# Kernel tuning notes

Hardware: AMD Instinct MI355X
Metric: run time of the kernel (lower is better)

The kernel has to match this reference:

```python
import jax, jax.numpy as jnp
import numpy as np

B, N, F_IN, F_HID, F_OUT = 32, 1024, 512, 512, 512


def setup_inputs() -> dict:
    key = jax.random.key(0)
    ks = jax.random.split(key, 8)
    def xavier(k, fan_in, fan_out):
        bound = float(np.sqrt(6.0 / (fan_in + fan_out)))
        return jax.random.uniform(k, (fan_in, fan_out), jnp.float32, -bound, bound)
    return {
        "batch_graph": jax.random.normal(ks[0], (B, N, F_IN), jnp.float32),
        "adj": jax.random.uniform(ks[1], (B, N, N), jnp.float32),
        "W1": xavier(ks[2], F_IN, F_HID),
        "b1": jnp.zeros((F_HID,), jnp.float32),
        "W2": xavier(ks[3], F_HID, F_HID),
        "b2": jnp.zeros((F_HID,), jnp.float32),
        "W3": xavier(ks[4], F_HID, F_OUT),
        "b3": jnp.zeros((F_OUT,), jnp.float32),
    }


def _gcn_layer(x, adj, W, b):
    # support = X @ W ; out = A @ support + b  (per graph in the batch)
    support = jnp.einsum("bnf,fh->bnh", x, W)
    return jnp.einsum("bnm,bmh->bnh", adj, support) + b


def reference(batch_graph, adj, W1, b1, W2, b2, W3, b3):
    # Block-diagonal big_adj @ big_graph is exactly a batched per-graph matmul:
    # the zero off-diagonal blocks contribute nothing, so math is identical.
    # Dropout is identity at inference (eval mode).
    x = jax.nn.relu(_gcn_layer(batch_graph, adj, W1, b1))
    x = jax.nn.relu(_gcn_layer(x, adj, W2, b2))
    out = _gcn_layer(x, adj, W3, b3)  # [B, N, F_OUT]
    return out
```

## Files before the change

kernel.cpp:

```cpp
#include <hip/hip_runtime.h>
#include <hip/hip_bf16.h>


typedef __attribute__((ext_vector_type(8))) short bf16x8s;
typedef __attribute__((ext_vector_type(4))) float f32x4;
typedef __attribute__((ext_vector_type(4))) unsigned short us4;
typedef __attribute__((ext_vector_type(8))) unsigned short us8;

__device__ __forceinline__ unsigned short f2bf(float f) {
    unsigned u = __builtin_bit_cast(unsigned, f);
    u += 0x7fffu + ((u >> 16) & 1u);
    return (unsigned short)(u >> 16);
}

__device__ __forceinline__ void async16(const unsigned short* g, unsigned short* l) {
    __builtin_amdgcn_global_load_lds(
        (const __attribute__((address_space(1))) unsigned int*)g,
        (__attribute__((address_space(3))) unsigned int*)l, 16, 0, 0);
}

#define MFMA_(d, va, vb) d = __builtin_amdgcn_mfma_f32_16x16x32_bf16(va, vb, d, 0, 0, 0)

__global__ void prep(const float* __restrict__ x0, unsigned short* __restrict__ P0, long n4,
                     const float* __restrict__ W1, const float* __restrict__ W2,
                     const float* __restrict__ W3, unsigned short* __restrict__ WT1,
                     unsigned short* __restrict__ WT2, unsigned short* __restrict__ WT3,
                     int F) {
    long i = (long)blockIdx.x * blockDim.x + threadIdx.x;
    long stride = (long)gridDim.x * blockDim.x;
    for (long k = i; k < n4; k += stride) {
        float4 v = ((const float4*)x0)[k];
        us4 o;
        o.x = f2bf(v.x); o.y = f2bf(v.y); o.z = f2bf(v.z); o.w = f2bf(v.w);
        ((us4*)P0)[k] = o;
    }
    const long FF = (long)F * F;
    for (long k = i; k < 3 * FF; k += stride) {
        int w = (int)(k / FF);
        long idx = k % FF;
        int r = (int)(idx % F);
        int c = (int)(idx / F);
        const float* W = (w == 0) ? W1 : (w == 1) ? W2 : W3;
        unsigned short* WT = (w == 0) ? WT1 : (w == 1) ? WT2 : WT3;
        WT[idx] = f2bf(W[(size_t)r * F + c]);
    }
}

__global__ void cvt_f32_bf16(const float* __restrict__ in, unsigned short* __restrict__ out, long n4) {
    long i = (long)blockIdx.x * blockDim.x + threadIdx.x;
    long stride = (long)gridDim.x * blockDim.x;
    for (; i < n4; i += stride) {
        float4 v = ((const float4*)in)[i];
        us4 o;
        o.x = f2bf(v.x); o.y = f2bf(v.y); o.z = f2bf(v.z); o.w = f2bf(v.w);
        ((us4*)out)[i] = o;
    }
}

template<bool RELU, bool OUT_F32>
__global__ __launch_bounds__(512, 2)
void gemm256(const unsigned short* __restrict__ A,
             const unsigned short* __restrict__ BT,
             void* __restrict__ Cout,
             const float* __restrict__ bias,
             int M, int N, int K,
             long sA, long sBT, long sC)
{
    __shared__ unsigned short Lraw[65536];

    const int t    = threadIdx.x;
    const int lane = t & 63;
    const int wv   = t >> 6;
    const int wm   = wv >> 2;
    const int wn   = wv & 3;
    const int fr   = lane & 15;
    const int fk   = (lane >> 4) * 8;
    const int r4   = (lane >> 4) * 4;

    const int tilesN = N >> 8;
    const int bpb    = (M >> 8) * tilesN;
    const int cpx = gridDim.x >> 3;
    const int lb  = (blockIdx.x & 7) * cpx + (blockIdx.x >> 3);
    const int bat = lb / bpb;
    const int tt  = lb % bpb;
    const int m0  = (tt / tilesN) << 8;
    const int n0  = (tt % tilesN) << 8;

    const unsigned short* Ab = A  + (size_t)bat * sA  + (size_t)m0 * K;
    const unsigned short* Bb = BT + (size_t)bat * sBT + (size_t)n0 * K;

    int srow[2], scol[2], lo[2];
#pragma unroll
    for (int r = 0; r < 2; ++r) {
        int c   = r * 512 + t;
        srow[r] = c >> 3;
        scol[r] = ((c & 7) * 8) ^ ((srow[r] & 7) << 3);
        lo[r]   = c * 8;
    }

    auto stageA = [&](int kt, int h) {
        unsigned short* base = Lraw + (kt & 1) * 16384;
#pragma unroll
        for (int r = 0; r < 2; ++r)
            async16(Ab + (size_t)(h * 128 + srow[r]) * K + kt * 64 + scol[r],
                    base + h * 8192 + lo[r]);
    };
    auto stageB = [&](int kt, int h) {
        unsigned short* base = Lraw + 32768 + (kt & 1) * 16384;
#pragma unroll
        for (int r = 0; r < 2; ++r)
            async16(Bb + (size_t)(h * 128 + srow[r]) * K + kt * 64 + scol[r],
                    base + h * 8192 + lo[r]);
    };
    auto rdA = [&](int buf, int mf, int kkj) -> bf16x8s {
        int row = wm * 128 + mf * 16 + fr;
        int e   = (kkj * 32 + fk) ^ ((row & 7) << 3);
        return *(const bf16x8s*)&Lraw[buf * 16384 + row * 64 + e];
    };
    auto rdB = [&](int buf, int nf, int kkj) -> bf16x8s {
        int row = wn * 64 + nf * 16 + fr;
        int e   = (kkj * 32 + fk) ^ ((row & 7) << 3);
        return *(const bf16x8s*)&Lraw[32768 + buf * 16384 + row * 64 + e];
    };

    const int nt = K >> 6;

    f32x4 acc[8][4];
#pragma unroll
    for (int i = 0; i < 8; ++i)
#pragma unroll
        for (int j = 0; j < 4; ++j) acc[i][j] = f32x4{0.f, 0.f, 0.f, 0.f};

    bf16x8s aP[4], aB[4], aC[4], bX[4], bY[4];

    stageA(0, 0); stageB(0, 0); stageA(0, 1); stageB(0, 1);
    asm volatile("s_waitcnt vmcnt(0)" ::: "memory");
    __builtin_amdgcn_s_barrier();
#pragma unroll
    for (int m = 0; m < 4; ++m) aP[m] = rdA(0, m, 0);
#pragma unroll
    for (int n = 0; n < 4; ++n) bX[n] = rdB(0, n, 0);

    for (int it = 0; it < nt; ++it) {
        const int cur  = it & 1;
        const int nxt  = cur ^ 1;
        const bool more = (it + 1 < nt);

        __builtin_amdgcn_s_barrier();
#pragma unroll
        for (int m = 0; m < 4; ++m) aB[m] = rdA(cur, m + 4, 0);
        if (more) { stageA(it + 1, 0); stageB(it + 1, 0); }
        __builtin_amdgcn_s_setprio(1);
#pragma unroll
        for (int m = 0; m < 4; ++m)
#pragma unroll
            for (int n = 0; n < 4; ++n) MFMA_(acc[m][n], aP[m], bX[n]);
        __builtin_amdgcn_s_setprio(0);

        __builtin_amdgcn_s_barrier();
#pragma unroll
        for (int m = 0; m < 4; ++m) aC[m] = rdA(cur, m, 1);
#pragma unroll
        for (int n = 0; n < 4; ++n) bY[n] = rdB(cur, n, 1);
        if (more) { stageA(it + 1, 1); stageB(it + 1, 1); }
        __builtin_amdgcn_s_setprio(1);
#pragma unroll
        for (int m = 0; m < 4; ++m)
#pragma unroll
            for (int n = 0; n < 4; ++n) MFMA_(acc[m + 4][n], aB[m], bX[n]);
        __builtin_amdgcn_s_setprio(0);

        __builtin_amdgcn_s_barrier();
#pragma unroll
        for (int m = 0; m < 4; ++m) aB[m] = rdA(cur, m + 4, 1);
        __builtin_amdgcn_s_setprio(1);
#pragma unroll
        for (int m = 0; m < 4; ++m)
#pragma unroll
            for (int n = 0; n < 4; ++n) MFMA_(acc[m][n], aC[m], bY[n]);
        __builtin_amdgcn_s_setprio(0);

        if (more) {
            asm volatile("s_waitcnt vmcnt(0)" ::: "memory");
            __builtin_amdgcn_s_barrier();
#pragma unroll
            for (int m = 0; m < 4; ++m) aP[m] = rdA(nxt, m, 0);
#pragma unroll
            for (int n = 0; n < 4; ++n) bX[n] = rdB(nxt, n, 0);
        }
        __builtin_amdgcn_s_setprio(1);
#pragma unroll
        for (int m = 0; m < 4; ++m)
#pragma unroll
            for (int n = 0; n < 4; ++n) MFMA_(acc[m + 4][n], aB[m], bY[n]);
        __builtin_amdgcn_s_setprio(0);
    }

    __syncthreads();

    const int R0 = m0 + wm * 128;
    const int C0 = n0 + wn * 64;
    float bv[4];
#pragma unroll
    for (int j = 0; j < 4; ++j)
        bv[j] = bias ? bias[C0 + j * 16 + fr] : 0.f;

    if (OUT_F32) {
        float* Cb = (float*)Cout + (size_t)bat * sC;
#pragma unroll
        for (int j = 0; j < 4; ++j)
#pragma unroll
            for (int i = 0; i < 8; ++i)
#pragma unroll
                for (int e = 0; e < 4; ++e) {
                    float v = acc[i][j][e] + bv[j];
                    if (RELU) v = fmaxf(v, 0.f);
                    Cb[(size_t)(R0 + i * 16 + r4 + e) * N + C0 + j * 16 + fr] = v;
                }
    } else {
        unsigned short* sl = Lraw + wv * 8192;
#pragma unroll
        for (int i = 0; i < 8; ++i)
#pragma unroll
            for (int j = 0; j < 4; ++j)
#pragma unroll
                for (int e = 0; e < 4; ++e) {
                    float v = acc[i][j][e] + bv[j];
                    if (RELU) v = fmaxf(v, 0.f);
                    const int row = i * 16 + r4 + e;
                    const int col = j * 16 + fr;
                    sl[row * 64 + (col ^ ((row & 7) << 3))] = f2bf(v);
                }
        unsigned short* Cb = (unsigned short*)Cout + (size_t)bat * sC;
#pragma unroll
        for (int rr = 0; rr < 16; ++rr) {
            const int row = rr * 8 + (lane >> 3);
            const int k8  = lane & 7;
            us8 v = *(const us8*)&sl[row * 64 + ((k8 ^ (row & 7)) << 3)];
            *(us8*)&Cb[(size_t)(R0 + row) * N + C0 + k8 * 8] = v;
        }
    }
}

extern "C" void kernel_launch(void* const* d_in, const int* in_sizes, int n_in,
                              void* d_out, int out_size, void* d_ws, size_t ws_size,
                              hipStream_t stream) {
    constexpr int B = 32, N = 1024, F = 512;

    const float* x0f  = (const float*)d_in[0];
    const float* adjf = (const float*)d_in[1];
    const float* W1 = (const float*)d_in[2];
    const float* b1 = (const float*)d_in[3];
    const float* W2 = (const float*)d_in[4];
    const float* b2 = (const float*)d_in[5];
    const float* W3 = (const float*)d_in[6];
    const float* b3 = (const float*)d_in[7];

    unsigned short* ws   = (unsigned short*)d_ws;
    unsigned short* adjb = ws;
    unsigned short* P0   = adjb + (size_t)B * N * N;
    unsigned short* P1   = P0 + (size_t)B * N * F;
    unsigned short* PT   = P1 + (size_t)B * N * F;
    unsigned short* WT1  = PT + (size_t)B * N * F;
    unsigned short* WT2  = WT1 + (size_t)F * F;
    unsigned short* WT3  = WT2 + (size_t)F * F;

    prep<<<2048, 256, 0, stream>>>(x0f, P0, (long)B * N * F / 4,
                                   W1, W2, W3, WT1, WT2, WT3, F);
    cvt_f32_bf16<<<2048, 256, 0, stream>>>(adjf, adjb, (long)B * N * N / 4);

    const int grid = 256;
    const long sX = (long)N * F;
    const long sAd = (long)N * N;

    gemm256<false, false><<<grid, 512, 0, stream>>>(WT1,  P0, PT, nullptr, F, N, F, 0,  sX, sX);
    gemm256<true,  false><<<grid, 512, 0, stream>>>(adjb, PT, P1, b1,      N, F, N, sAd, sX, sX);
    gemm256<false, false><<<grid, 512, 0, stream>>>(WT2,  P1, PT, nullptr, F, N, F, 0,  sX, sX);
    gemm256<true,  false><<<grid, 512, 0, stream>>>(adjb, PT, P0, b2,      N, F, N, sAd, sX, sX);
    gemm256<false, false><<<grid, 512, 0, stream>>>(WT3,  P0, PT, nullptr, F, N, F, 0,  sX, sX);
    gemm256<false, true ><<<grid, 512, 0, stream>>>(adjb, PT, (float*)d_out, b3, N, F, N, sAd, sX, sX);
}
```

Baseline: 256.3 us.

## Fuse all GCN layers and adj conversion into one persistent kernel with flag sync

Replaces the six GEMM launches and the separate adjacency conversion kernel with a single persistent 256-block kernel. Per-tile completion flags let each adj@support GEMM start consuming K-chunks as soon as the producing X@W tiles finish. The fp32-to-bf16 adjacency conversion is interleaved after the first X@W GEMM, and grid-wide barriers separate the layers. This aims to remove launch gaps and tail idle time and to overlap the conversion with compute. It relies on all 256 blocks being co-resident (2 per CU) to avoid deadlock, and it adds spin-wait and atomic overhead.

Measured after the change: 737.7 us. 188% more time.

```diff
diff --git a/kernel.cpp b/kernel.cpp
--- a/kernel.cpp
+++ b/kernel.cpp
@@ -20,6 +20,10 @@
 }
 
 #define MFMA_(d, va, vb) d = __builtin_amdgcn_mfma_f32_16x16x32_bf16(va, vb, d, 0, 0, 0)
+
+__global__ void zero_sync(unsigned* s, int n) {
+    for (int i = threadIdx.x; i < n; i += 256) s[i] = 0;
+}
 
 __global__ void prep(const float* __restrict__ x0, unsigned short* __restrict__ P0, long n4,
                      const float* __restrict__ W1, const float* __restrict__ W2,
@@ -46,28 +50,34 @@
     }
 }
 
-__global__ void cvt_f32_bf16(const float* __restrict__ in, unsigned short* __restrict__ out, long n4) {
-    long i = (long)blockIdx.x * blockDim.x + threadIdx.x;
-    long stride = (long)gridDim.x * blockDim.x;
-    for (; i < n4; i += stride) {
-        float4 v = ((const float4*)in)[i];
-        us4 o;
-        o.x = f2bf(v.x); o.y = f2bf(v.y); o.z = f2bf(v.z); o.w = f2bf(v.w);
-        ((us4*)out)[i] = o;
-    }
-}
-
-template<bool RELU, bool OUT_F32>
-__global__ __launch_bounds__(512, 2)
-void gemm256(const unsigned short* __restrict__ A,
-             const unsigned short* __restrict__ BT,
-             void* __restrict__ Cout,
-             const float* __restrict__ bias,
-             int M, int N, int K,
-             long sA, long sBT, long sC)
+__device__ __forceinline__ void waitge(unsigned* p, unsigned tgt, int t) {
+    if (t == 0) {
+        while (__hip_atomic_load(p, __ATOMIC_ACQUIRE, __HIP_MEMORY_SCOPE_AGENT) < tgt)
+            __builtin_amdgcn_s_sleep(2);
+    }
+    __syncthreads();
+    __builtin_amdgcn_sched_barrier(0);
+}
+
+__device__ __forceinline__ void gbar(unsigned* slot, unsigned nb, int t) {
+    __syncthreads();
+    if (t == 0) {
+        __hip_atomic_fetch_add(slot, 1u, __ATOMIC_ACQ_REL, __HIP_MEMORY_SCOPE_AGENT);
+        while (__hip_atomic_load(slot, __ATOMIC_ACQUIRE, __HIP_MEMORY_SCOPE_AGENT) < nb)
+            __builtin_amdgcn_s_sleep(2);
+    }
+    __syncthreads();
+    __builtin_amdgcn_sched_barrier(0);
+}
+
+__device__ __forceinline__ void gemm_core(
+    unsigned short* Lraw,
+    const unsigned short* __restrict__ A, const unsigned short* __restrict__ BT,
+    void* __restrict__ Cout, const float* __restrict__ bias,
+    int N, int K, int lgTN, long sA, long sBT, long sC,
+    bool relu, bool outf32,
+    unsigned* wTf, unsigned* wCvt, unsigned* sTf, int lb)
 {
-    __shared__ unsigned short Lraw[65536];
-
     const int t    = threadIdx.x;
     const int lane = t & 63;
     const int wv   = t >> 6;
@@ -77,14 +87,11 @@
     const int fk   = (lane >> 4) * 8;
     const int r4   = (lane >> 4) * 4;
 
-    const int tilesN = N >> 8;
-    const int bpb    = (M >> 8) * tilesN;
-    const int cpx = gridDim.x >> 3;
-    const int lb  = (blockIdx.x & 7) * cpx + (blockIdx.x >> 3);
-    const int bat = lb / bpb;
-    const int tt  = lb % bpb;
-    const int m0  = (tt / tilesN) << 8;
-    const int n0  = (tt % tilesN) << 8;
+    const int bat = lb >> 3;
+    const int tt  = lb & 7;
+    const int m0  = (tt >> lgTN) << 8;
+    const int n0  = (tt & ((1 << lgTN) - 1)) << 8;
+    const int nfeat = n0 >> 8;
 
     const unsigned short* Ab = A  + (size_t)bat * sA  + (size_t)m0 * K;
     const unsigned short* Bb = BT + (size_t)bat * sBT + (size_t)n0 * K;
@@ -133,6 +140,9 @@
 
     bf16x8s aP[4], aB[4], aC[4], bX[4], bY[4];
 
+    if (wCvt) waitge(&wCvt[bat], 8, t);
+    if (wTf)  waitge(&wTf[bat * 8 + nfeat * 4 + 0], 1, t);
+
     stageA(0, 0); stageB(0, 0); stageA(0, 1); stageB(0, 1);
     asm volatile("s_waitcnt vmcnt(0)" ::: "memory");
     __builtin_amdgcn_s_barrier();
@@ -146,6 +156,9 @@
         const int nxt  = cur ^ 1;
         const bool more = (it + 1 < nt);
 
+        if (wTf && more && (((it + 1) & 3) == 0))
+            waitge(&wTf[bat * 8 + nfeat * 4 + ((it + 1) >> 2)], 1, t);
+
         __builtin_amdgcn_s_barrier();
 #pragma unroll
         for (int m = 0; m < 4; ++m) aB[m] = rdA(cur, m + 4, 0);
@@ -205,7 +218,7 @@
     for (int j = 0; j < 4; ++j)
         bv[j] = bias ? bias[C0 + j * 16 + fr] : 0.f;
 
-    if (OUT_F32) {
+    if (outf32) {
         float* Cb = (float*)Cout + (size_t)bat * sC;
 #pragma unroll
         for (int j = 0; j < 4; ++j)
@@ -214,7 +227,7 @@
 #pragma unroll
                 for (int e = 0; e < 4; ++e) {
                     float v = acc[i][j][e] + bv[j];
-                    if (RELU) v = fmaxf(v, 0.f);
+                    if (relu) v = fmaxf(v, 0.f);
                     Cb[(size_t)(R0 + i * 16 + r4 + e) * N + C0 + j * 16 + fr] = v;
                 }
     } else {
@@ -226,7 +239,7 @@
 #pragma unroll
                 for (int e = 0; e < 4; ++e) {
                     float v = acc[i][j][e] + bv[j];
-                    if (RELU) v = fmaxf(v, 0.f);
+                    if (relu) v = fmaxf(v, 0.f);
                     const int row = i * 16 + r4 + e;
                     const int col = j * 16 + fr;
                     sl[row * 64 + (col ^ ((row & 7) << 3))] = f2bf(v);
@@ -239,6 +252,69 @@
             us8 v = *(const us8*)&sl[row * 64 + ((k8 ^ (row & 7)) << 3)];
             *(us8*)&Cb[(size_t)(R0 + row) * N + C0 + k8 * 8] = v;
         }
+    }
+
+    __syncthreads();
+    if (sTf && t == 0)
+        __hip_atomic_fetch_add(&sTf[lb], 1u, __ATOMIC_RELEASE, __HIP_MEMORY_SCOPE_AGENT);
+}
+
+__global__ __launch_bounds__(512, 2)
+void mega(const float* __restrict__ adjf,
+          unsigned short* __restrict__ adjb,
+          unsigned short* __restrict__ P0, unsigned short* __restrict__ P1,
+          unsigned short* __restrict__ PT,
+          const unsigned short* __restrict__ WT1, const unsigned short* __restrict__ WT2,
+          const unsigned short* __restrict__ WT3,
+          const float* __restrict__ b1, const float* __restrict__ b2,
+          const float* __restrict__ b3,
+          float* __restrict__ dout,
+          unsigned* __restrict__ sync)
+{
+    __shared__ unsigned short Lraw[65536];
+
+    const int t   = threadIdx.x;
+    const int cpx = 32;
+    const int lb  = ((int)blockIdx.x & 7) * cpx + ((int)blockIdx.x >> 3);
+
+    unsigned* slots  = sync;
+    unsigned* tflags = sync + 16;
+    unsigned* cvtcnt = sync + 16 + 768;
+
+    const long sX  = 1024L * 512;
+    const long sAd = 1024L * 1024;
+
+    const unsigned short* Wt[3]  = {WT1, WT2, WT3};
+    const unsigned short* Xin[3] = {P0, P1, P0};
+    const float* bb[3]           = {b1, b2, b3};
+
+    for (int l = 0; l < 3; ++l) {
+        gemm_core(Lraw, Wt[l], Xin[l], PT, nullptr,
+                  1024, 512, 2, 0, sX, sX,
+                  false, false, nullptr, nullptr, &tflags[l * 256], lb);
+
+        if (l == 0) {
+            const int bc = lb >> 3, s = lb & 7;
+            const float4* src = (const float4*)adjf + ((size_t)bc * 262144 + (size_t)s * 32768);
+            us4* dst = (us4*)adjb + ((size_t)bc * 262144 + (size_t)s * 32768);
+            for (int i = t; i < 32768; i += 512) {
+                float4 v = src[i];
+                us4 o;
+                o.x = f2bf(v.x); o.y = f2bf(v.y); o.z = f2bf(v.z); o.w = f2bf(v.w);
+                dst[i] = o;
+            }
+            __syncthreads();
+            if (t == 0)
+                __hip_atomic_fetch_add(&cvtcnt[bc], 1u, __ATOMIC_RELEASE, __HIP_MEMORY_SCOPE_AGENT);
+        }
+
+        void* outp = (l == 0) ? (void*)P1 : (l == 1) ? (void*)P0 : (void*)dout;
+        gemm_core(Lraw, adjb, PT, outp, bb[l],
+                  512, 1024, 1, sAd, sX, sX,
+                  (l < 2), (l == 2),
+                  &tflags[l * 256], (l == 0) ? cvtcnt : nullptr, nullptr, lb);
+
+        if (l < 2) gbar(&slots[l], 256, t);
     }
 }
 
@@ -264,19 +340,12 @@
     unsigned short* WT1  = PT + (size_t)B * N * F;
     unsigned short* WT2  = WT1 + (size_t)F * F;
     unsigned short* WT3  = WT2 + (size_t)F * F;
-
+    unsigned* sync       = (unsigned*)(WT3 + (size_t)F * F);
+    constexpr int SYNC_WORDS = 16 + 3 * 256 + 32;
+
+    zero_sync<<<1, 256, 0, stream>>>(sync, SYNC_WORDS);
     prep<<<2048, 256, 0, stream>>>(x0f, P0, (long)B * N * F / 4,
                                    W1, W2, W3, WT1, WT2, WT3, F);
-    cvt_f32_bf16<<<2048, 256, 0, stream>>>(adjf, adjb, (long)B * N * N / 4);
-
-    const int grid = 256;
-    const long sX = (long)N * F;
-    const long sAd = (long)N * N;
-
-    gemm256<false, false><<<grid, 512, 0, stream>>>(WT1,  P0, PT, nullptr, F, N, F, 0,  sX, sX);
-    gemm256<true,  false><<<grid, 512, 0, stream>>>(adjb, PT, P1, b1,      N, F, N, sAd, sX, sX);
-    gemm256<false, false><<<grid, 512, 0, stream>>>(WT2,  P1, PT, nullptr, F, N, F, 0,  sX, sX);
-    gemm256<true,  false><<<grid, 512, 0, stream>>>(adjb, PT, P0, b2,      N, F, N, sAd, sX, sX);
-    gemm256<false, false><<<grid, 512, 0, stream>>>(WT3,  P0, PT, nullptr, F, N, F, 0,  sX, sX);
-    gemm256<false, true ><<<grid, 512, 0, stream>>>(adjb, PT, (float*)d_out, b3, N, F, N, sAd, sX, sX);
-}
+    mega<<<256, 512, 0, stream>>>(adjf, adjb, P0, P1, PT, WT1, WT2, WT3,
+                                  b1, b2, b3, (float*)d_out, sync);
+}
```

## Triple-buffer B tiles to prefetch two k-steps ahead; fuse adj conversion into prep

Applied to the files above, without the earlier changes.

The GEMM kernel now gives the B operand three LDS buffers and issues its loads two k-iterations ahead. The waits become partial (vmcnt(4)) rather than full drains, so more global latency is hidden behind MFMA work. The adjacency fp32-to-bf16 conversion moves into the prep kernel, which removes one launch. The cost is LDS per block growing from 128KB to 160KB, which may cut the occupancy of 2 blocks per CU and makes the wait-count bookkeeping more fragile.

Result: no change. 256.0 us (-0.1%).

```diff
diff --git a/kernel.cpp b/kernel.cpp
--- a/kernel.cpp
+++ b/kernel.cpp
@@ -22,12 +22,19 @@
 #define MFMA_(d, va, vb) d = __builtin_amdgcn_mfma_f32_16x16x32_bf16(va, vb, d, 0, 0, 0)
 
 __global__ void prep(const float* __restrict__ x0, unsigned short* __restrict__ P0, long n4,
+                     const float* __restrict__ adjf, unsigned short* __restrict__ adjb, long na4,
                      const float* __restrict__ W1, const float* __restrict__ W2,
                      const float* __restrict__ W3, unsigned short* __restrict__ WT1,
                      unsigned short* __restrict__ WT2, unsigned short* __restrict__ WT3,
                      int F) {
     long i = (long)blockIdx.x * blockDim.x + threadIdx.x;
     long stride = (long)gridDim.x * blockDim.x;
+    for (long k = i; k < na4; k += stride) {
+        float4 v = ((const float4*)adjf)[k];
+        us4 o;
+        o.x = f2bf(v.x); o.y = f2bf(v.y); o.z = f2bf(v.z); o.w = f2bf(v.w);
+        ((us4*)adjb)[k] = o;
+    }
     for (long k = i; k < n4; k += stride) {
         float4 v = ((const float4*)x0)[k];
         us4 o;
@@ -46,17 +53,6 @@
     }
 }
 
-__global__ void cvt_f32_bf16(const float* __restrict__ in, unsigned short* __restrict__ out, long n4) {
-    long i = (long)blockIdx.x * blockDim.x + threadIdx.x;
-    long stride = (long)gridDim.x * blockDim.x;
-    for (; i < n4; i += stride) {
-        float4 v = ((const float4*)in)[i];
-        us4 o;
-        o.x = f2bf(v.x); o.y = f2bf(v.y); o.z = f2bf(v.z); o.w = f2bf(v.w);
-        ((us4*)out)[i] = o;
-    }
-}
-
 template<bool RELU, bool OUT_F32>
 __global__ __launch_bounds__(512, 2)
 void gemm256(const unsigned short* __restrict__ A,
@@ -66,7 +62,7 @@
              int M, int N, int K,
              long sA, long sBT, long sC)
 {
-    __shared__ unsigned short Lraw[65536];
+    __shared__ unsigned short Lraw[81920];
 
     const int t    = threadIdx.x;
     const int lane = t & 63;
@@ -105,12 +101,14 @@
             async16(Ab + (size_t)(h * 128 + srow[r]) * K + kt * 64 + scol[r],
                     base + h * 8192 + lo[r]);
     };
-    auto stageB = [&](int kt, int h) {
-        unsigned short* base = Lraw + 32768 + (kt & 1) * 16384;
-#pragma unroll
-        for (int r = 0; r < 2; ++r)
-            async16(Bb + (size_t)(h * 128 + srow[r]) * K + kt * 64 + scol[r],
-                    base + h * 8192 + lo[r]);
+    auto stageB = [&](int buf, int kt) {
+        unsigned short* base = Lraw + 32768 + buf * 16384;
+#pragma unroll
+        for (int h = 0; h < 2; ++h)
+#pragma unroll
+            for (int r = 0; r < 2; ++r)
+                async16(Bb + (size_t)(h * 128 + srow[r]) * K + kt * 64 + scol[r],
+                        base + h * 8192 + lo[r]);
     };
     auto rdA = [&](int buf, int mf, int kkj) -> bf16x8s {
         int row = wm * 128 + mf * 16 + fr;
@@ -133,23 +131,31 @@
 
     bf16x8s aP[4], aB[4], aC[4], bX[4], bY[4];
 
-    stageA(0, 0); stageB(0, 0); stageA(0, 1); stageB(0, 1);
-    asm volatile("s_waitcnt vmcnt(0)" ::: "memory");
+    stageA(0, 0); stageA(0, 1);
+    stageB(0, 0);
+    if (nt > 1) {
+        stageB(1, 1);
+        asm volatile("s_waitcnt vmcnt(4)" ::: "memory");
+    } else {
+        asm volatile("s_waitcnt vmcnt(0)" ::: "memory");
+    }
     __builtin_amdgcn_s_barrier();
 #pragma unroll
     for (int m = 0; m < 4; ++m) aP[m] = rdA(0, m, 0);
 #pragma unroll
     for (int n = 0; n < 4; ++n) bX[n] = rdB(0, n, 0);
 
+    int bc = 0;
     for (int it = 0; it < nt; ++it) {
-        const int cur  = it & 1;
-        const int nxt  = cur ^ 1;
-        const bool more = (it + 1 < nt);
+        const int cur = it & 1;
+        const int bn1 = (bc == 2) ? 0 : bc + 1;
+        const int bn2 = (bn1 == 2) ? 0 : bn1 + 1;
+        const bool m1 = (it + 1 < nt), m2 = (it + 2 < nt);
 
         __builtin_amdgcn_s_barrier();
 #pragma unroll
         for (int m = 0; m < 4; ++m) aB[m] = rdA(cur, m + 4, 0);
-        if (more) { stageA(it + 1, 0); stageB(it + 1, 0); }
+        if (m1) stageA(it + 1, 0);
         __builtin_amdgcn_s_setprio(1);
 #pragma unroll
         for (int m = 0; m < 4; ++m)
@@ -161,8 +167,8 @@
 #pragma unroll
         for (int m = 0; m < 4; ++m) aC[m] = rdA(cur, m, 1);
 #pragma unroll
-        for (int n = 0; n < 4; ++n) bY[n] = rdB(cur, n, 1);
-        if (more) { stageA(it + 1, 1); stageB(it + 1, 1); }
+        for (int n = 0; n < 4; ++n) bY[n] = rdB(bc, n, 1);
+        if (m1) stageA(it + 1, 1);
         __builtin_amdgcn_s_setprio(1);
 #pragma unroll
         for (int m = 0; m < 4; ++m)
@@ -173,6 +179,7 @@
         __builtin_amdgcn_s_barrier();
 #pragma unroll
         for (int m = 0; m < 4; ++m) aB[m] = rdA(cur, m + 4, 1);
+        if (m2) stageB(bn2, it + 2);
         __builtin_amdgcn_s_setprio(1);
 #pragma unroll
         for (int m = 0; m < 4; ++m)
@@ -180,13 +187,14 @@
             for (int n = 0; n < 4; ++n) MFMA_(acc[m][n], aC[m], bY[n]);
         __builtin_amdgcn_s_setprio(0);
 
-        if (more) {
-            asm volatile("s_waitcnt vmcnt(0)" ::: "memory");
+        if (m1) {
+            if (m2) asm volatile("s_waitcnt vmcnt(4)" ::: "memory");
+            else    asm volatile("s_waitcnt vmcnt(0)" ::: "memory");
             __builtin_amdgcn_s_barrier();
 #pragma unroll
-            for (int m = 0; m < 4; ++m) aP[m] = rdA(nxt, m, 0);
-#pragma unroll
-            for (int n = 0; n < 4; ++n) bX[n] = rdB(nxt, n, 0);
+            for (int m = 0; m < 4; ++m) aP[m] = rdA(cur ^ 1, m, 0);
+#pragma unroll
+            for (int n = 0; n < 4; ++n) bX[n] = rdB(bn1, n, 0);
         }
         __builtin_amdgcn_s_setprio(1);
 #pragma unroll
@@ -194,6 +202,7 @@
 #pragma unroll
             for (int n = 0; n < 4; ++n) MFMA_(acc[m + 4][n], aB[m], bY[n]);
         __builtin_amdgcn_s_setprio(0);
+        bc = bn1;
     }
 
     __syncthreads();
@@ -266,8 +275,8 @@
     unsigned short* WT3  = WT2 + (size_t)F * F;
 
     prep<<<2048, 256, 0, stream>>>(x0f, P0, (long)B * N * F / 4,
+                                   adjf, adjb, (long)B * N * N / 4,
                                    W1, W2, W3, WT1, WT2, WT3, F);
-    cvt_f32_bf16<<<2048, 256, 0, stream>>>(adjf, adjb, (long)B * N * N / 4);
 
     const int grid = 256;
     const long sX = (long)N * F;
```
